# Kernel optimization log

Hardware: AMD Instinct MI355X
Metric: run time of the kernel (lower is better)

Reference implementation:

```python
import jax, jax.numpy as jnp
import numpy as np

INV_TEMPERATURE = 0.125  # 1/sqrt(head_dim=64)


def setup_inputs() -> dict:
    key = jax.random.key(0)
    kq, kk, kv, kp, km = jax.random.split(key, 5)
    B, H, S, D = 8, 8, 2048, 64
    q = jax.random.normal(kq, (B, H, S, D), dtype=jnp.float32)
    k = jax.random.normal(kk, (B, H, S, D), dtype=jnp.float32)
    v = jax.random.normal(kv, (B, H, S, D), dtype=jnp.float32)
    pos_scores = jax.random.normal(kp, (1, H, S, S), dtype=jnp.float32)
    mask = jax.random.uniform(km, (1, 1, S, S), dtype=jnp.float32)
    return {"q": q, "k": k, "v": v, "pos_scores": pos_scores, "mask": mask}


def reference(q, k, v, pos_scores, mask):
    # sim = (q k^T) * inv_temp + pos_scores, then multiplicative mask
    sim = jnp.einsum('bhid,bhjd->bhij', q, k) * INV_TEMPERATURE
    sim = mask * (sim + pos_scores)
    attn = jax.nn.softmax(sim, axis=-1)
    out = jnp.einsum('bhij,bhjd->bhid', attn, v)
    return out
```

## Files before the change

### kernel.cpp

```cpp
#include <hip/hip_runtime.h>

constexpr int SEQ = 2048;
constexpr int HD  = 64;
constexpr int NH  = 8;
constexpr int NB  = 8;
constexpr int BM  = 64;
constexpr int BN  = 64;
constexpr int KST = 72;
constexpr float INV_T = 0.125f;
constexpr float LOG2E = 1.4426950408889634f;

typedef __attribute__((ext_vector_type(8))) short bf16x8;
typedef __attribute__((ext_vector_type(8))) short s16x8;
typedef __attribute__((ext_vector_type(4))) short s16x4;
typedef __attribute__((ext_vector_type(4))) float f32x4;
typedef __attribute__((ext_vector_type(4))) unsigned u32x4;

__device__ __forceinline__ short f2bf(float f) {
  unsigned u = __builtin_bit_cast(unsigned, f);
  u += 0x7fffu + ((u >> 16) & 1u);
  return (short)(u >> 16);
}
__device__ __forceinline__ float bf2f(short s) {
  unsigned u = ((unsigned)(unsigned short)s) << 16;
  return __builtin_bit_cast(float, u);
}
__device__ __forceinline__ float fast_exp2(float x) {
#if __has_builtin(__builtin_amdgcn_exp2f)
  return __builtin_amdgcn_exp2f(x);
#else
  return exp2f(x);
#endif
}

__global__ __launch_bounds__(256)
void prep_kv(const float* __restrict__ k, const float* __restrict__ v,
             unsigned short* __restrict__ kb, unsigned short* __restrict__ vt)
{
  __shared__ unsigned short t[HD * KST];
  const int bh = blockIdx.y, jt = blockIdx.x, tid = threadIdx.x;
  const size_t base = (size_t)bh * SEQ * HD + (size_t)jt * BN * HD;

  {
    const float* kp = k + base + 16 * tid;
    unsigned short ko[16];
    for (int e = 0; e < 4; ++e) {
      f32x4 x = *(const f32x4*)(kp + 4 * e);
      for (int c = 0; c < 4; ++c) ko[4 * e + c] = (unsigned short)f2bf(x[c]);
    }
    *(s16x8*)(kb + base + 16 * tid)     = *(const s16x8*)&ko[0];
    *(s16x8*)(kb + base + 16 * tid + 8) = *(const s16x8*)&ko[8];
  }
  {
    const float* vp = v + base + 16 * tid;
    const int j = tid >> 2, d0 = (tid & 3) * 16;
    for (int e = 0; e < 4; ++e) {
      f32x4 x = *(const f32x4*)(vp + 4 * e);
      for (int c = 0; c < 4; ++c) t[(d0 + 4 * e + c) * KST + j] = (unsigned short)f2bf(x[c]);
    }
  }
  __syncthreads();
  {
    const int d = tid >> 2, ch = tid & 3;
    const size_t ob = (size_t)bh * HD * SEQ + (size_t)d * SEQ + jt * BN + ch * 16;
    *(s16x8*)(vt + ob)     = *(const s16x8*)&t[d * KST + ch * 16];
    *(s16x8*)(vt + ob + 8) = *(const s16x8*)&t[d * KST + ch * 16 + 8];
  }
}

__global__ __launch_bounds__(256)
void prep_pack(const float* __restrict__ pos, const float* __restrict__ mask,
               unsigned* __restrict__ pk)
{
  const int w  = blockIdx.x * 256 + threadIdx.x;
  const int lq = w & 15;
  const int i  = (w >> 4) & 2047;
  const int jh = w >> 15;
  const int jt = jh & 31, h = jh >> 5;
  u32x4 o;
  for (int sub = 0; sub < 4; ++sub) {
    const int j = jt * 64 + sub * 16 + lq;
    float m = mask[(size_t)i * SEQ + j];
    float p = pos[((size_t)h * SEQ + i) * SEQ + j];
    unsigned mb = (unsigned)(unsigned short)f2bf(m * LOG2E);
    unsigned pb = (unsigned)(unsigned short)f2bf(m * p * LOG2E);
    o[sub] = (mb << 16) | pb;
  }
  *(u32x4*)(pk + (size_t)4 * w) = o;
}

__global__ __launch_bounds__(256, 8)
void attn_main(const float* __restrict__ q, const unsigned short* __restrict__ kb,
               const unsigned short* __restrict__ vt, const unsigned* __restrict__ pk,
               float* __restrict__ out)
{
  __shared__ unsigned short lds_k[BN * KST];
  __shared__ unsigned short lds_v[HD * KST];

  const int bh = blockIdx.y, h = bh & (NH - 1);
  const int i0 = blockIdx.x * BM;
  const int tid = threadIdx.x, wave = tid >> 6, lane = tid & 63;
  const int quad = lane >> 4, lq = lane & 15;

  bf16x8 aq[2];
  {
    const float* qp = q + ((size_t)bh * SEQ + i0 + wave * 16 + lq) * HD + quad * 8;
    for (int k0 = 0; k0 < 2; ++k0) {
      f32x4 x = *(const f32x4*)(qp + k0 * 32);
      f32x4 y = *(const f32x4*)(qp + k0 * 32 + 4);
      for (int c = 0; c < 4; ++c) {
        aq[k0][c]     = f2bf(x[c] * INV_T);
        aq[k0][4 + c] = f2bf(y[c] * INV_T);
      }
    }
  }

  f32x4 oacc[4];
  for (int d = 0; d < 4; ++d) oacc[d] = (f32x4){0.f, 0.f, 0.f, 0.f};
  float lrun[4] = {0.f, 0.f, 0.f, 0.f};

  const int lw = (tid >> 3) * KST + (tid & 7) * 8;
  const unsigned short* kgb = kb + (size_t)bh * SEQ * HD + 8 * tid;
  const unsigned short* vgb = vt + (size_t)bh * HD * SEQ + (tid >> 3) * SEQ + (tid & 7) * 8;
  const unsigned* mpb = pk + ((((size_t)h * 32) * SEQ + (i0 + wave * 16 + quad * 4)) * 16 + lq) * 4;

  for (int jt = 0; jt < SEQ / BN; ++jt) {
    __syncthreads();
    s16x8 kx0 = *(const s16x8*)(kgb + jt * 4096);
    s16x8 kx1 = *(const s16x8*)(kgb + jt * 4096 + 2048);
    s16x8 vx0 = *(const s16x8*)(vgb + jt * 64);
    s16x8 vx1 = *(const s16x8*)(vgb + jt * 64 + 32 * SEQ);
    *(s16x8*)&lds_k[lw]            = kx0;
    *(s16x8*)&lds_k[lw + 32 * KST] = kx1;
    *(s16x8*)&lds_v[lw]            = vx0;
    *(s16x8*)&lds_v[lw + 32 * KST] = vx1;
    __syncthreads();

    f32x4 sa[4];
    for (int s = 0; s < 4; ++s) sa[s] = (f32x4){0.f, 0.f, 0.f, 0.f};
    for (int k0 = 0; k0 < 2; ++k0)
      for (int s = 0; s < 4; ++s) {
        bf16x8 bk = *(const bf16x8*)&lds_k[(s * 16 + lq) * KST + k0 * 32 + quad * 8];
        sa[s] = __builtin_amdgcn_mfma_f32_16x16x32_bf16(aq[k0], bk, sa[s], 0, 0, 0);
      }
    __syncthreads();

    const unsigned* mp = mpb + (size_t)jt * (SEQ * 64);
    for (int r = 0; r < 4; ++r) {
      u32x4 u = *(const u32x4*)(mp + r * 64);
      float ps = 0.f;
      for (int s = 0; s < 4; ++s) {
        float mf = __builtin_bit_cast(float, u[s] & 0xffff0000u);
        float mq = __builtin_bit_cast(float, u[s] << 16);
        float p  = fast_exp2(fmaf(mf, sa[s][r], mq));
        unsigned pu = __builtin_bit_cast(unsigned, p);
        lds_k[wave * (16 * KST) + (quad * 4 + r) * KST + s * 16 + lq] = (unsigned short)(pu >> 16);
        ps += __builtin_bit_cast(float, pu & 0xffff0000u);
      }
      for (int off = 1; off < 16; off <<= 1) ps += __shfl_xor(ps, off);
      lrun[r] += ps;
    }
    asm volatile("s_waitcnt lgkmcnt(0)" ::: "memory");

    for (int k0 = 0; k0 < 2; ++k0) {
      bf16x8 ap = *(const bf16x8*)&lds_k[wave * (16 * KST) + lq * KST + k0 * 32 + quad * 8];
      for (int d = 0; d < 4; ++d) {
        bf16x8 bv = *(const bf16x8*)&lds_v[(d * 16 + lq) * KST + k0 * 32 + quad * 8];
        oacc[d] = __builtin_amdgcn_mfma_f32_16x16x32_bf16(ap, bv, oacc[d], 0, 0, 0);
      }
    }
  }

  for (int r = 0; r < 4; ++r) {
    const float inv = 1.0f / lrun[r];
    float* orow = out + ((size_t)bh * SEQ + i0 + wave * 16 + quad * 4 + r) * HD + lq;
    for (int d = 0; d < 4; ++d) orow[d * 16] = oacc[d][r] * inv;
  }
}

__global__ __launch_bounds__(256, 2)
void attn_fused(const float* __restrict__ q, const float* __restrict__ kk,
                const float* __restrict__ vv, const float* __restrict__ pos,
                const float* __restrict__ mask, float* __restrict__ out)
{
  __shared__ short lds_k[BN * KST];
  __shared__ short lds_v[HD * KST];
  __shared__ short lds_p[4][16 * KST];
  const int bh = blockIdx.y, h = bh & (NH - 1);
  const int i0 = blockIdx.x * BM;
  const int tid = threadIdx.x, wave = tid >> 6, lane = tid & 63;
  const int quad = lane >> 4, lq = lane & 15;
  bf16x8 aq[2];
  {
    const float* qp = q + ((size_t)bh * SEQ + i0 + wave * 16 + lq) * HD + quad * 8;
    for (int k0 = 0; k0 < 2; ++k0) {
      f32x4 x = *(const f32x4*)(qp + k0 * 32);
      f32x4 y = *(const f32x4*)(qp + k0 * 32 + 4);
      for (int j = 0; j < 4; ++j) { aq[k0][j] = f2bf(x[j] * INV_T); aq[k0][4 + j] = f2bf(y[j] * INV_T); }
    }
  }
  f32x4 oacc[4];
  for (int d = 0; d < 4; ++d) oacc[d] = (f32x4){0.f, 0.f, 0.f, 0.f};
  float mrun[4] = {-INFINITY, -INFINITY, -INFINITY, -INFINITY};
  float lrun[4] = {0.f, 0.f, 0.f, 0.f};
  const size_t kvbase = (size_t)bh * SEQ * HD;
  for (int jt = 0; jt < SEQ / BN; ++jt) {
    const int j0 = jt * BN;
    __syncthreads();
    for (int e = 0; e < 4; ++e) {
      int idx = e * 256 + tid, j = idx >> 4, d4 = (idx & 15) << 2;
      f32x4 kf = *(const f32x4*)(kk + kvbase + (size_t)(j0 + j) * HD + d4);
      s16x4 ks;
      for (int c = 0; c < 4; ++c) ks[c] = f2bf(kf[c]);
      *(s16x4*)&lds_k[j * KST + d4] = ks;
      f32x4 vf = *(const f32x4*)(vv + kvbase + (size_t)(j0 + j) * HD + d4);
      for (int c = 0; c < 4; ++c) lds_v[(d4 + c) * KST + j] = f2bf(vf[c]);
    }
    __syncthreads();
    float mk[4][4], pz[4][4];
    for (int r = 0; r < 4; ++r) {
      const int i = i0 + wave * 16 + quad * 4 + r;
      const float* mrow = mask + (size_t)i * SEQ + j0 + lq;
      const float* prow = pos + ((size_t)h * SEQ + i) * SEQ + j0 + lq;
      for (int s = 0; s < 4; ++s) { mk[r][s] = mrow[s * 16]; pz[r][s] = prow[s * 16]; }
    }
    f32x4 sa[4];
    for (int s = 0; s < 4; ++s) sa[s] = (f32x4){0.f, 0.f, 0.f, 0.f};
    for (int k0 = 0; k0 < 2; ++k0)
      for (int s = 0; s < 4; ++s) {
        bf16x8 bk = *(const bf16x8*)&lds_k[(s * 16 + lq) * KST + k0 * 32 + quad * 8];
        sa[s] = __builtin_amdgcn_mfma_f32_16x16x32_bf16(aq[k0], bk, sa[s], 0, 0, 0);
      }
    for (int r = 0; r < 4; ++r) {
      float s0 = mk[r][0] * (sa[0][r] + pz[r][0]);
      float s1 = mk[r][1] * (sa[1][r] + pz[r][1]);
      float s2 = mk[r][2] * (sa[2][r] + pz[r][2]);
      float s3 = mk[r][3] * (sa[3][r] + pz[r][3]);
      float rm = fmaxf(fmaxf(s0, s1), fmaxf(s2, s3));
      for (int off = 1; off < 16; off <<= 1) rm = fmaxf(rm, __shfl_xor(rm, off));
      float mn = fmaxf(mrun[r], rm);
      float al = __expf(mrun[r] - mn);
      mrun[r] = mn;
      short p0 = f2bf(__expf(s0 - mn)), p1 = f2bf(__expf(s1 - mn));
      short p2 = f2bf(__expf(s2 - mn)), p3 = f2bf(__expf(s3 - mn));
      float ps = bf2f(p0) + bf2f(p1) + bf2f(p2) + bf2f(p3);
      for (int off = 1; off < 16; off <<= 1) ps += __shfl_xor(ps, off);
      lrun[r] = lrun[r] * al + ps;
      for (int d = 0; d < 4; ++d) oacc[d][r] *= al;
      short* pr = &lds_p[wave][(quad * 4 + r) * KST + lq];
      pr[0] = p0; pr[16] = p1; pr[32] = p2; pr[48] = p3;
    }
    asm volatile("s_waitcnt lgkmcnt(0)" ::: "memory");
    for (int k0 = 0; k0 < 2; ++k0) {
      bf16x8 ap = *(const bf16x8*)&lds_p[wave][lq * KST + k0 * 32 + quad * 8];
      for (int d = 0; d < 4; ++d) {
        bf16x8 bv = *(const bf16x8*)&lds_v[(d * 16 + lq) * KST + k0 * 32 + quad * 8];
        oacc[d] = __builtin_amdgcn_mfma_f32_16x16x32_bf16(ap, bv, oacc[d], 0, 0, 0);
      }
    }
  }
  for (int r = 0; r < 4; ++r) {
    const int i = i0 + wave * 16 + quad * 4 + r;
    const float inv = 1.0f / lrun[r];
    float* orow = out + ((size_t)bh * SEQ + i) * HD + lq;
    for (int d = 0; d < 4; ++d) orow[d * 16] = oacc[d][r] * inv;
  }
}

extern "C" void kernel_launch(void* const* d_in, const int* in_sizes, int n_in,
                              void* d_out, int out_size, void* d_ws, size_t ws_size,
                              hipStream_t stream) {
  const float* q    = (const float*)d_in[0];
  const float* k    = (const float*)d_in[1];
  const float* v    = (const float*)d_in[2];
  const float* pos  = (const float*)d_in[3];
  const float* mask = (const float*)d_in[4];
  float* out = (float*)d_out;

  const size_t kv_elems = (size_t)NB * NH * SEQ * HD;
  const size_t kb_bytes = kv_elems * 2;
  const size_t pk_dwords = (size_t)NH * SEQ * SEQ;
  const size_t need = 2 * kb_bytes + pk_dwords * 4;

  if (ws_size >= need) {
    unsigned short* kb = (unsigned short*)d_ws;
    unsigned short* vt = (unsigned short*)((char*)d_ws + kb_bytes);
    unsigned*       pk = (unsigned*)((char*)d_ws + 2 * kb_bytes);
    prep_kv<<<dim3(SEQ / BN, NB * NH), dim3(256), 0, stream>>>(k, v, kb, vt);
    prep_pack<<<dim3((int)(pk_dwords / 4 / 256)), dim3(256), 0, stream>>>(pos, mask, pk);
    attn_main<<<dim3(SEQ / BM, NB * NH), dim3(256), 0, stream>>>(q, kb, vt, pk, out);
  } else {
    attn_fused<<<dim3(SEQ / BM, NB * NH), dim3(256), 0, stream>>>(q, k, v, pos, mask, out);
  }
}
```

Baseline: 498.1 us.

## Split pos/mask packing into separate bf16 buffers and prefetch next K/V tile

Replaces the combined per-head packed mask*pos dword buffer with a per-head bf16 pos buffer and a single shared bf16 mask buffer, which shrinks the preprocessed data read per head and reuses the mask across heads. The K/V global loads for the next tile are issued into registers before the current tile's compute so that load latency overlaps the matmuls. The per-row sum shuffle reduction moves out of the loop to the epilogue, and the P tile uses a narrower LDS stride read as two 4-element loads. The exp argument now computes mask*(s+pos) with separate bf16 rounding, which changes numerics slightly and adds register pressure.

```diff
diff --git a/kernel.cpp b/kernel.cpp
--- a/kernel.cpp
+++ b/kernel.cpp
@@ -7,22 +7,23 @@
 constexpr int BM  = 64;
 constexpr int BN  = 64;
 constexpr int KST = 72;
+constexpr int PST = 68;
 constexpr float INV_T = 0.125f;
 constexpr float LOG2E = 1.4426950408889634f;
 
 typedef __attribute__((ext_vector_type(8))) short bf16x8;
 typedef __attribute__((ext_vector_type(8))) short s16x8;
 typedef __attribute__((ext_vector_type(4))) short s16x4;
+typedef __attribute__((ext_vector_type(4))) unsigned short us4;
 typedef __attribute__((ext_vector_type(4))) float f32x4;
-typedef __attribute__((ext_vector_type(4))) unsigned u32x4;
 
 __device__ __forceinline__ short f2bf(float f) {
   unsigned u = __builtin_bit_cast(unsigned, f);
   u += 0x7fffu + ((u >> 16) & 1u);
   return (short)(u >> 16);
 }
-__device__ __forceinline__ float bf2f(short s) {
-  unsigned u = ((unsigned)(unsigned short)s) << 16;
+__device__ __forceinline__ float bf2f(unsigned short s) {
+  unsigned u = ((unsigned)s) << 16;
   return __builtin_bit_cast(float, u);
 }
 __device__ __forceinline__ float fast_exp2(float x) {
@@ -40,7 +41,6 @@
   __shared__ unsigned short t[HD * KST];
   const int bh = blockIdx.y, jt = blockIdx.x, tid = threadIdx.x;
   const size_t base = (size_t)bh * SEQ * HD + (size_t)jt * BN * HD;
-
   {
     const float* kp = k + base + 16 * tid;
     unsigned short ko[16];
@@ -69,30 +69,44 @@
 }
 
 __global__ __launch_bounds__(256)
-void prep_pack(const float* __restrict__ pos, const float* __restrict__ mask,
-               unsigned* __restrict__ pk)
-{
-  const int w  = blockIdx.x * 256 + threadIdx.x;
-  const int lq = w & 15;
-  const int i  = (w >> 4) & 2047;
-  const int jh = w >> 15;
-  const int jt = jh & 31, h = jh >> 5;
-  u32x4 o;
-  for (int sub = 0; sub < 4; ++sub) {
-    const int j = jt * 64 + sub * 16 + lq;
-    float m = mask[(size_t)i * SEQ + j];
-    float p = pos[((size_t)h * SEQ + i) * SEQ + j];
-    unsigned mb = (unsigned)(unsigned short)f2bf(m * LOG2E);
-    unsigned pb = (unsigned)(unsigned short)f2bf(m * p * LOG2E);
-    o[sub] = (mb << 16) | pb;
-  }
-  *(u32x4*)(pk + (size_t)4 * w) = o;
+void prep_mask(const float* __restrict__ mask, unsigned short* __restrict__ mp)
+{
+  const int w = blockIdx.x * 256 + threadIdx.x;
+  const int W = w << 2;
+  const int lq0 = W & 15;
+  const int i   = (W >> 4) & 2047;
+  const int jt  = W >> 15;
+  const float* src = mask + (size_t)i * SEQ + jt * 64;
+  unsigned short o[16];
+  for (int c = 0; c < 4; ++c)
+    for (int s = 0; s < 4; ++s)
+      o[c * 4 + s] = (unsigned short)f2bf(src[s * 16 + lq0 + c] * LOG2E);
+  *(s16x8*)(mp + (size_t)4 * W)     = *(const s16x8*)&o[0];
+  *(s16x8*)(mp + (size_t)4 * W + 8) = *(const s16x8*)&o[8];
+}
+
+__global__ __launch_bounds__(256)
+void prep_pos(const float* __restrict__ pos, unsigned short* __restrict__ pp)
+{
+  const size_t w = (size_t)blockIdx.x * 256 + threadIdx.x;
+  const int W = (int)(w << 2);
+  const int lq0 = W & 15;
+  const int i   = (W >> 4) & 2047;
+  const int jt  = (W >> 15) & 31;
+  const int h   = (int)(w >> 18);
+  const float* src = pos + ((size_t)h * SEQ + i) * SEQ + jt * 64;
+  unsigned short o[16];
+  for (int c = 0; c < 4; ++c)
+    for (int s = 0; s < 4; ++s)
+      o[c * 4 + s] = (unsigned short)f2bf(src[s * 16 + lq0 + c]);
+  *(s16x8*)(pp + (size_t)4 * W)     = *(const s16x8*)&o[0];
+  *(s16x8*)(pp + (size_t)4 * W + 8) = *(const s16x8*)&o[8];
 }
 
 __global__ __launch_bounds__(256, 8)
 void attn_main(const float* __restrict__ q, const unsigned short* __restrict__ kb,
-               const unsigned short* __restrict__ vt, const unsigned* __restrict__ pk,
-               float* __restrict__ out)
+               const unsigned short* __restrict__ vt, const unsigned short* __restrict__ posp,
+               const unsigned short* __restrict__ maskp, float* __restrict__ out)
 {
   __shared__ unsigned short lds_k[BN * KST];
   __shared__ unsigned short lds_v[HD * KST];
@@ -122,19 +136,29 @@
   const int lw = (tid >> 3) * KST + (tid & 7) * 8;
   const unsigned short* kgb = kb + (size_t)bh * SEQ * HD + 8 * tid;
   const unsigned short* vgb = vt + (size_t)bh * HD * SEQ + (tid >> 3) * SEQ + (tid & 7) * 8;
-  const unsigned* mpb = pk + ((((size_t)h * 32) * SEQ + (i0 + wave * 16 + quad * 4)) * 16 + lq) * 4;
+  const int irow = i0 + wave * 16 + quad * 4;
+  const unsigned short* posb = posp + (((size_t)h * 65536 + irow) * 16 + lq) * 4;
+  const unsigned short* mkb  = maskp + ((size_t)irow * 16 + lq) * 4;
+  unsigned short* pwave = &lds_k[wave * (16 * PST)];
+
+  s16x8 kx0 = *(const s16x8*)(kgb);
+  s16x8 kx1 = *(const s16x8*)(kgb + 2048);
+  s16x8 vx0 = *(const s16x8*)(vgb);
+  s16x8 vx1 = *(const s16x8*)(vgb + 32 * SEQ);
 
   for (int jt = 0; jt < SEQ / BN; ++jt) {
     __syncthreads();
-    s16x8 kx0 = *(const s16x8*)(kgb + jt * 4096);
-    s16x8 kx1 = *(const s16x8*)(kgb + jt * 4096 + 2048);
-    s16x8 vx0 = *(const s16x8*)(vgb + jt * 64);
-    s16x8 vx1 = *(const s16x8*)(vgb + jt * 64 + 32 * SEQ);
     *(s16x8*)&lds_k[lw]            = kx0;
     *(s16x8*)&lds_k[lw + 32 * KST] = kx1;
     *(s16x8*)&lds_v[lw]            = vx0;
     *(s16x8*)&lds_v[lw + 32 * KST] = vx1;
     __syncthreads();
+
+    const int jn = (jt + 1) & 31;
+    kx0 = *(const s16x8*)(kgb + jn * 4096);
+    kx1 = *(const s16x8*)(kgb + jn * 4096 + 2048);
+    vx0 = *(const s16x8*)(vgb + jn * 64);
+    vx1 = *(const s16x8*)(vgb + jn * 64 + 32 * SEQ);
 
     f32x4 sa[4];
     for (int s = 0; s < 4; ++s) sa[s] = (f32x4){0.f, 0.f, 0.f, 0.f};
@@ -145,25 +169,28 @@
       }
     __syncthreads();
 
-    const unsigned* mp = mpb + (size_t)jt * (SEQ * 64);
+    const unsigned short* pp = posb + jt * 131072;
+    const unsigned short* mm = mkb  + jt * 131072;
     for (int r = 0; r < 4; ++r) {
-      u32x4 u = *(const u32x4*)(mp + r * 64);
+      us4 pb4 = *(const us4*)(pp + r * 64);
+      us4 mb4 = *(const us4*)(mm + r * 64);
       float ps = 0.f;
       for (int s = 0; s < 4; ++s) {
-        float mf = __builtin_bit_cast(float, u[s] & 0xffff0000u);
-        float mq = __builtin_bit_cast(float, u[s] << 16);
-        float p  = fast_exp2(fmaf(mf, sa[s][r], mq));
+        float p = fast_exp2(bf2f(mb4[s]) * (sa[s][r] + bf2f(pb4[s])));
         unsigned pu = __builtin_bit_cast(unsigned, p);
-        lds_k[wave * (16 * KST) + (quad * 4 + r) * KST + s * 16 + lq] = (unsigned short)(pu >> 16);
+        pwave[(quad * 4 + r) * PST + s * 16 + lq] = (unsigned short)(pu >> 16);
         ps += __builtin_bit_cast(float, pu & 0xffff0000u);
       }
-      for (int off = 1; off < 16; off <<= 1) ps += __shfl_xor(ps, off);
       lrun[r] += ps;
     }
     asm volatile("s_waitcnt lgkmcnt(0)" ::: "memory");
 
     for (int k0 = 0; k0 < 2; ++k0) {
-      bf16x8 ap = *(const bf16x8*)&lds_k[wave * (16 * KST) + lq * KST + k0 * 32 + quad * 8];
+      const unsigned short* pr = &pwave[lq * PST + k0 * 32 + quad * 8];
+      s16x4 lo = *(const s16x4*)pr;
+      s16x4 hi = *(const s16x4*)(pr + 4);
+      bf16x8 ap;
+      for (int c = 0; c < 4; ++c) { ap[c] = lo[c]; ap[4 + c] = hi[c]; }
       for (int d = 0; d < 4; ++d) {
         bf16x8 bv = *(const bf16x8*)&lds_v[(d * 16 + lq) * KST + k0 * 32 + quad * 8];
         oacc[d] = __builtin_amdgcn_mfma_f32_16x16x32_bf16(ap, bv, oacc[d], 0, 0, 0);
@@ -172,7 +199,9 @@
   }
 
   for (int r = 0; r < 4; ++r) {
-    const float inv = 1.0f / lrun[r];
+    float l = lrun[r];
+    for (int off = 1; off < 16; off <<= 1) l += __shfl_xor(l, off);
+    const float inv = 1.0f / l;
     float* orow = out + ((size_t)bh * SEQ + i0 + wave * 16 + quad * 4 + r) * HD + lq;
     for (int d = 0; d < 4; ++d) orow[d * 16] = oacc[d][r] * inv;
   }
@@ -243,7 +272,7 @@
       mrun[r] = mn;
       short p0 = f2bf(__expf(s0 - mn)), p1 = f2bf(__expf(s1 - mn));
       short p2 = f2bf(__expf(s2 - mn)), p3 = f2bf(__expf(s3 - mn));
-      float ps = bf2f(p0) + bf2f(p1) + bf2f(p2) + bf2f(p3);
+      float ps = bf2f((unsigned short)p0) + bf2f((unsigned short)p1) + bf2f((unsigned short)p2) + bf2f((unsigned short)p3);
       for (int off = 1; off < 16; off <<= 1) ps += __shfl_xor(ps, off);
       lrun[r] = lrun[r] * al + ps;
       for (int d = 0; d < 4; ++d) oacc[d][r] *= al;
@@ -277,18 +306,20 @@
   const float* mask = (const float*)d_in[4];
   float* out = (float*)d_out;
 
-  const size_t kv_elems = (size_t)NB * NH * SEQ * HD;
-  const size_t kb_bytes = kv_elems * 2;
-  const size_t pk_dwords = (size_t)NH * SEQ * SEQ;
-  const size_t need = 2 * kb_bytes + pk_dwords * 4;
+  const size_t kb_bytes   = (size_t)NB * NH * SEQ * HD * 2;
+  const size_t posp_bytes = (size_t)NH * SEQ * SEQ * 2;
+  const size_t mask_bytes = (size_t)SEQ * SEQ * 2;
+  const size_t need = 2 * kb_bytes + posp_bytes + mask_bytes;
 
   if (ws_size >= need) {
     unsigned short* kb = (unsigned short*)d_ws;
     unsigned short* vt = (unsigned short*)((char*)d_ws + kb_bytes);
-    unsigned*       pk = (unsigned*)((char*)d_ws + 2 * kb_bytes);
+    unsigned short* pp = (unsigned short*)((char*)d_ws + 2 * kb_bytes);
+    unsigned short* mp = (unsigned short*)((char*)d_ws + 2 * kb_bytes + posp_bytes);
     prep_kv<<<dim3(SEQ / BN, NB * NH), dim3(256), 0, stream>>>(k, v, kb, vt);
-    prep_pack<<<dim3((int)(pk_dwords / 4 / 256)), dim3(256), 0, stream>>>(pos, mask, pk);
-    attn_main<<<dim3(SEQ / BM, NB * NH), dim3(256), 0, stream>>>(q, kb, vt, pk, out);
+    prep_mask<<<dim3(1024), dim3(256), 0, stream>>>(mask, mp);
+    prep_pos<<<dim3(8192), dim3(256), 0, stream>>>(pos, pp);
+    attn_main<<<dim3(SEQ / BM, NB * NH), dim3(256), 0, stream>>>(q, kb, vt, pp, mp, out);
   } else {
     attn_fused<<<dim3(SEQ / BM, NB * NH), dim3(256), 0, stream>>>(q, k, v, pos, mask, out);
   }
```

New measurement: 681.0 us. 1.37x slower.
